# Kernel tuning notes

Measured on AMD Instinct MI355X. Metric: run time of the kernel, lower is better.

Reference implementation:

```python
import jax, jax.numpy as jnp
import numpy as np

DIM = 1024
N_HEADS = 16
HEAD_DIM = DIM // N_HEADS
LORA_DIM = 16
B, T = 4, 1024


def _rope(x):
    # x: [B, H, T, D] with D even; rotate first/second halves (torch impl style)
    D = x.shape[-1]
    half = D // 2
    theta = 1.0 / (10000.0 ** (jnp.arange(0, D, 2, dtype=jnp.float32) / D))  # [D/2]
    pos = jnp.arange(x.shape[-2], dtype=jnp.float32)                         # [T]
    pt = pos[:, None] * theta[None, :]                                       # [T, D/2]
    sin, cos = jnp.sin(pt), jnp.cos(pt)
    xr, xi = x[..., :half], x[..., half:]
    return jnp.concatenate([xr * cos - xi * sin, xr * sin + xi * cos], axis=-1)


def setup_inputs() -> dict:
    key = jax.random.key(0)
    ks = jax.random.split(key, 16)
    def n(k, shape, std=0.02):
        return jax.random.normal(k, shape, jnp.float32) * std
    return {
        "x": jax.random.normal(ks[0], (B, T, DIM), jnp.float32),
        "q_w": n(ks[1], (DIM, DIM)),
        "k_w": n(ks[2], (DIM, DIM)),
        "v_w": n(ks[3], (DIM, DIM)),
        "q_a": n(ks[4], (LORA_DIM, DIM), 0.001),
        "q_b": n(ks[5], (DIM, LORA_DIM), 0.001),
        "q_l": jax.random.normal(ks[6], (DIM,), jnp.float32),
        "k_a": n(ks[7], (LORA_DIM, DIM), 0.001),
        "k_b": n(ks[8], (DIM, LORA_DIM), 0.001),
        "k_l": jax.random.normal(ks[9], (DIM,), jnp.float32),
        "v_a": n(ks[10], (LORA_DIM, DIM), 0.001),
        "v_b": n(ks[11], (DIM, LORA_DIM), 0.001),
        "v_l": jax.random.normal(ks[12], (DIM,), jnp.float32),
        "proj_w": n(ks[13], (DIM, DIM)),
        "proj_b": n(ks[14], (DIM,)),
    }


def reference(x, q_w, k_w, v_w, q_a, q_b, q_l, k_a, k_b, k_l,
              v_a, v_b, v_l, proj_w, proj_b):
    Bb, Tt, C = x.shape
    # token shift: xx[t] = x[t-1], xx[0] = 0 (ZeroPad2d((0,0,1,-1)))
    xx = jnp.pad(x, ((0, 0), (1, 0), (0, 0)))[:, :Tt]
    xxx = xx - x

    def lora(a, b, lam):
        return lam + jnp.tanh(x @ a.T) @ b.T  # [B,T,C]

    q = (x + xxx * lora(q_a, q_b, q_l)) @ q_w.T
    k = (x + xxx * lora(k_a, k_b, k_l)) @ k_w.T
    v = (x + xxx * lora(v_a, v_b, v_l)) @ v_w.T

    def split_heads(t):
        return t.reshape(Bb, Tt, N_HEADS, HEAD_DIM).transpose(0, 2, 1, 3)  # [B,H,T,D]

    q = _rope(split_heads(q))
    k = _rope(split_heads(k))
    v = split_heads(v)

    scale = 1.0 / np.sqrt(HEAD_DIM).astype(np.float32)
    scores = jnp.einsum('bhqd,bhkd->bhqk', q, k) * scale
    causal = jnp.tril(jnp.ones((Tt, Tt), dtype=bool))
    scores = jnp.where(causal, scores, jnp.float32(-1e30))
    att = jax.nn.softmax(scores, axis=-1)
    out = jnp.einsum('bhqk,bhkd->bhqd', att, v)
    out = out.transpose(0, 2, 1, 3).reshape(Bb, Tt, C)
    return out @ proj_w.T + proj_b
```

## Files before the change

### kernel.cpp

```cpp
#include <hip/hip_runtime.h>
#include <hip/hip_bf16.h>

typedef __hip_bfloat16 bf16;
typedef __attribute__((ext_vector_type(8))) short bf16x8;
typedef __attribute__((ext_vector_type(4))) float f32x4;

typedef const __attribute__((address_space(1))) unsigned int* gp_t;
typedef __attribute__((address_space(3))) unsigned int* lp_t;

__device__ __forceinline__ bf16 tobf(float f) { return __float2bfloat16(f); }
__device__ __forceinline__ float tof(bf16 h) { return __bfloat162float(h); }

__device__ __forceinline__ short bfbits(float f) {
    bf16 h = __float2bfloat16(f);
    return *reinterpret_cast<short*>(&h);
}
__device__ __forceinline__ bf16x8 pack8(float4 a, float4 b) {
    bf16x8 r;
    r[0] = bfbits(a.x); r[1] = bfbits(a.y); r[2] = bfbits(a.z); r[3] = bfbits(a.w);
    r[4] = bfbits(b.x); r[5] = bfbits(b.y); r[6] = bfbits(b.z); r[7] = bfbits(b.w);
    return r;
}

__device__ __forceinline__ void gload_lds16(const void* g, void* l) {
    __builtin_amdgcn_global_load_lds((gp_t)g, (lp_t)l, 16, 0, 0);
}

__global__ __launch_bounds__(256) void convert_w(const float* qw, const float* kw,
                                                 const float* vw, const float* pw,
                                                 bf16* dst) {
    int m = blockIdx.y;
    const float* src = m == 0 ? qw : (m == 1 ? kw : (m == 2 ? vw : pw));
    bf16* d = dst + (size_t)m * (1u << 20);
    int i = (blockIdx.x * 256 + threadIdx.x) * 4;
    float4 f = *(const float4*)(src + i);
    d[i + 0] = tobf(f.x);
    d[i + 1] = tobf(f.y);
    d[i + 2] = tobf(f.z);
    d[i + 3] = tobf(f.w);
}

__global__ __launch_bounds__(256) void lora_gate_fused(
    const float* x,
    const float* qa, const float* ka, const float* va,
    const float* qbw, const float* ql,
    const float* kbw, const float* kl,
    const float* vbw, const float* vl,
    bf16* xqo, bf16* xko, bf16* xvo) {
    const int XS = 1028;
    int row0 = blockIdx.x * 16;
    int t0 = row0 & 1023;
    int tid = threadIdx.x;
    int wave = tid >> 6, lane = tid & 63;
    int quad = lane >> 4, l16 = lane & 15;

    __shared__ float sx[17 * 1028];
    __shared__ float sT[16 * 48];

    {
        int prow = (row0 == 0) ? 0 : row0 - 1;
        for (int i = 0; i < 17; ++i) {
            int grow = (i == 0) ? prow : row0 + i - 1;
            gload_lds16(x + (size_t)grow * 1024 + wave * 256 + lane * 4,
                        &sx[i * XS + wave * 256]);
        }
    }
    __syncthreads();

    if (wave < 3) {
        const float* am = wave == 0 ? qa : (wave == 1 ? ka : va);
        f32x4 acc = (f32x4){0.f, 0.f, 0.f, 0.f};
#pragma unroll 4
        for (int k0 = 0; k0 < 1024; k0 += 32) {
            const float* xs = &sx[(1 + l16) * XS + k0 + quad * 8];
            bf16x8 af = pack8(*(const float4*)xs, *(const float4*)(xs + 4));
            const float* as = am + (size_t)l16 * 1024 + k0 + quad * 8;
            bf16x8 bf_ = pack8(*(const float4*)as, *(const float4*)(as + 4));
            acc = __builtin_amdgcn_mfma_f32_16x16x32_bf16(af, bf_, acc, 0, 0, 0);
        }
#pragma unroll
        for (int r = 0; r < 4; ++r)
            sT[(quad * 4 + r) * 48 + wave * 16 + l16] = tanhf(acc[r]);
    }
    __syncthreads();

#pragma unroll
    for (int u = 0; u < 4; ++u) {
        int d = tid + u * 256;
        float qbv[16], kbv[16], vbv[16];
#pragma unroll
        for (int p = 0; p < 4; ++p) {
            *(float4*)&qbv[p * 4] = *(const float4*)(qbw + (size_t)d * 16 + p * 4);
            *(float4*)&kbv[p * 4] = *(const float4*)(kbw + (size_t)d * 16 + p * 4);
            *(float4*)&vbv[p * 4] = *(const float4*)(vbw + (size_t)d * 16 + p * 4);
        }
        float qlv = ql[d], klv = kl[d], vlv = vl[d];
        float xp = (t0 == 0) ? 0.f : sx[0 * XS + d];
        for (int rr = 0; rr < 16; ++rr) {
            float xc = sx[(rr + 1) * XS + d];
            float dx = xp - xc;
            float gq = qlv, gk = klv, gv = vlv;
#pragma unroll
            for (int j = 0; j < 16; ++j) {
                gq += sT[rr * 48 + j] * qbv[j];
                gk += sT[rr * 48 + 16 + j] * kbv[j];
                gv += sT[rr * 48 + 32 + j] * vbv[j];
            }
            size_t o = (size_t)(row0 + rr) * 1024 + d;
            xqo[o] = tobf(xc + dx * gq);
            xko[o] = tobf(xc + dx * gk);
            xvo[o] = tobf(xc + dx * gv);
            xp = xc;
        }
    }
}

__global__ __launch_bounds__(256) void gemm128(
    const bf16* A0, const bf16* A1, const bf16* A2,
    const bf16* W0, const bf16* W1, const bf16* W2,
    bf16* C0, bf16* C1, bf16* C2,
    const float* bias, float* outF, int proj, int zcnt) {
    const int K = 1024;
    int ppx = (zcnt * 32) >> 3;
    int xcd = blockIdx.x & 7;
    int j = blockIdx.x >> 3;
    int pair = xcd * ppx + (j >> 3);
    int n0 = (j & 7) * 128;
    int bz = pair >> 5;
    int m0 = (pair & 31) * 128;

    const bf16* A = bz == 0 ? A0 : (bz == 1 ? A1 : A2);
    const bf16* W = bz == 0 ? W0 : (bz == 1 ? W1 : W2);
    bf16* C = bz == 0 ? C0 : (bz == 1 ? C1 : C2);

    __shared__ alignas(16) bf16 sA[2][64 * 64];
    __shared__ alignas(16) bf16 sB[2][64 * 64];

    int wave = threadIdx.x >> 6, lane = threadIdx.x & 63;
    int quad = lane >> 4, l16 = lane & 15;

    f32x4 acc[4][4];
#pragma unroll
    for (int i = 0; i < 4; i++)
#pragma unroll
        for (int j2 = 0; j2 < 4; j2++) acc[i][j2] = (f32x4){0.f, 0.f, 0.f, 0.f};

    int Rb0 = wave * 16 + (lane >> 3);
    int s0 = lane & 7;

    auto stage = [&](int k0, int bufi) {
#pragma unroll
        for (int p = 0; p < 2; p++) {
            int R = Rb0 + p * 8;
            int cs = s0 ^ (R & 7);
            int mr = 2 * R + (cs >> 2);
            int kc = (cs & 3) * 8;
            gload_lds16(A + (size_t)(m0 + mr) * K + k0 + kc, &sA[bufi][(wave * 16 + p * 8) * 64]);
            gload_lds16(W + (size_t)(n0 + mr) * K + k0 + kc, &sB[bufi][(wave * 16 + p * 8) * 64]);
        }
    };

    int mw = (wave >> 1) * 64, nw = (wave & 1) * 64;
    int slot = (((l16 & 1) << 2) | quad) ^ ((l16 >> 1) & 7);
    int abase = ((mw >> 1) + (l16 >> 1)) * 64 + slot * 8;
    int bbase = ((nw >> 1) + (l16 >> 1)) * 64 + slot * 8;

    stage(0, 0);
    for (int it = 0; it < 32; ++it) {
        __syncthreads();
        if (it + 1 < 32) stage((it + 1) * 32, (it + 1) & 1);
        const bf16* pa = sA[it & 1];
        const bf16* pb = sB[it & 1];
        bf16x8 af[4], bfr[4];
#pragma unroll
        for (int f = 0; f < 4; f++) {
            af[f] = *(const bf16x8*)&pa[abase + f * 512];
            bfr[f] = *(const bf16x8*)&pb[bbase + f * 512];
        }
#pragma unroll
        for (int i = 0; i < 4; i++)
#pragma unroll
            for (int j2 = 0; j2 < 4; j2++)
                acc[i][j2] = __builtin_amdgcn_mfma_f32_16x16x32_bf16(af[i], bfr[j2], acc[i][j2], 0, 0, 0);
    }

    if (proj) {
#pragma unroll
        for (int i = 0; i < 4; i++) {
            int mrow = m0 + mw + i * 16 + quad * 4;
#pragma unroll
            for (int j2 = 0; j2 < 4; j2++) {
                int col = n0 + nw + j2 * 16 + l16;
                float bv = bias[col];
#pragma unroll
                for (int r = 0; r < 4; r++)
                    outF[(size_t)(mrow + r) * 1024 + col] = acc[i][j2][r] + bv;
            }
        }
    } else if (bz < 2) {
        float sc = (bz == 0) ? 0.125f : 1.0f;
#pragma unroll
        for (int i = 0; i < 4; i++) {
            int mrow = m0 + mw + i * 16 + quad * 4;
#pragma unroll
            for (int j2 = 0; j2 < 2; j2++) {
                int d = j2 * 16 + l16;
                float theta = __expf(-(float)d * (9.210340371976184f / 32.0f));
                int col = n0 + nw + j2 * 16 + l16;
#pragma unroll
                for (int r = 0; r < 4; r++) {
                    int t = (mrow + r) & 1023;
                    float s, c;
                    sincosf((float)t * theta, &s, &c);
                    float xr = acc[i][j2][r], xi = acc[i][j2 + 2][r];
                    C[(size_t)(mrow + r) * 1024 + col] = tobf((xr * c - xi * s) * sc);
                    C[(size_t)(mrow + r) * 1024 + col + 32] = tobf((xr * s + xi * c) * sc);
                }
            }
        }
    } else {
#pragma unroll
        for (int i = 0; i < 4; i++) {
            int mrow = m0 + mw + i * 16 + quad * 4;
#pragma unroll
            for (int j2 = 0; j2 < 4; j2++) {
                int col = n0 + nw + j2 * 16 + l16;
#pragma unroll
                for (int r = 0; r < 4; r++)
                    C[(size_t)(mrow + r) * 1024 + col] = tobf(acc[i][j2][r]);
            }
        }
    }
}

__global__ __launch_bounds__(256) void v_transpose(const bf16* v, bf16* Vt) {
    int bh = blockIdx.x, tblk = blockIdx.y;
    int b = bh >> 4, h = bh & 15;
    int t0 = tblk * 64;
    int tid = threadIdx.x;

    __shared__ bf16 sv[64 * 65];
    {
        int r = tid >> 2;
        int c0 = (tid & 3) * 16;
        size_t g = ((size_t)(b * 1024 + t0 + r)) * 1024 + h * 64 + c0;
#pragma unroll
        for (int u = 0; u < 16; u++) sv[(c0 + u) * 65 + r] = v[g + u];
    }
    __syncthreads();
    {
        int d = tid >> 2;
        int tc = (tid & 3) * 16;
        size_t g = ((size_t)(bh * 64 + d)) * 1024 + t0 + tc;
#pragma unroll
        for (int u = 0; u < 16; u++) Vt[g + u] = sv[d * 65 + tc + u];
    }
}

__global__ __launch_bounds__(256) void attention(const bf16* Qm, const bf16* Km,
                                                 const bf16* Vt, bf16* attn) {
    int gid = blockIdx.x;
    int qblk = 15 - (gid >> 6);
    int bh = (((gid >> 3) & 7) << 3) | (gid & 7);
    int b = bh >> 4, h = bh & 15;
    int wave = threadIdx.x >> 6, lane = threadIdx.x & 63;
    int quad = lane >> 4, l16 = lane & 15;
    int m7 = l16 & 7;

    const bf16* Qb = Qm + (size_t)b * 1024 * 1024 + h * 64;
    const bf16* Kb = Km + (size_t)b * 1024 * 1024 + h * 64;
    const bf16* Vb = Vt + (size_t)bh * 64 * 1024;

    __shared__ alignas(16) bf16 sK[2][64 * 64];
    __shared__ alignas(16) bf16 sV[2][64 * 64];
    __shared__ alignas(16) bf16 sP[4][16 * 64];

    int srow = lane >> 3;
    int scol = ((lane & 7) ^ srow) * 8;

    auto stage = [&](int kt, int bufi) {
#pragma unroll
        for (int p = 0; p < 2; p++) {
            int rbase = p * 32 + wave * 8;
            gload_lds16(Kb + (size_t)(kt * 64 + rbase + srow) * 1024 + scol, &sK[bufi][rbase * 64]);
            gload_lds16(Vb + (size_t)(rbase + srow) * 1024 + kt * 64 + scol, &sV[bufi][rbase * 64]);
        }
    };

    int qrow0 = qblk * 64 + wave * 16;
    bf16x8 aq0 = *(const bf16x8*)&Qb[(size_t)(qrow0 + l16) * 1024 + quad * 8];
    bf16x8 aq1 = *(const bf16x8*)&Qb[(size_t)(qrow0 + l16) * 1024 + quad * 8 + 32];

    f32x4 o[4];
#pragma unroll
    for (int nt = 0; nt < 4; nt++) o[nt] = (f32x4){0.f, 0.f, 0.f, 0.f};
    float mrow[4], lrow[4];
#pragma unroll
    for (int r = 0; r < 4; r++) { mrow[r] = -3.0e38f; lrow[r] = 0.f; }

    stage(0, 0);

    int buf = 0;
    for (int kt = 0; kt <= qblk; ++kt, buf ^= 1) {
        __syncthreads();
        if (kt < qblk) stage(kt + 1, buf ^ 1);

        f32x4 S[4];
#pragma unroll
        for (int j = 0; j < 4; j++) {
            int row = j * 16 + l16;
            bf16x8 bk0 = *(const bf16x8*)&sK[buf][row * 64 + ((quad ^ m7) * 8)];
            bf16x8 bk1 = *(const bf16x8*)&sK[buf][row * 64 + (((quad + 4) ^ m7) * 8)];
            f32x4 z = __builtin_amdgcn_mfma_f32_16x16x32_bf16(aq0, bk0, (f32x4){0.f, 0.f, 0.f, 0.f}, 0, 0, 0);
            S[j] = __builtin_amdgcn_mfma_f32_16x16x32_bf16(aq1, bk1, z, 0, 0, 0);
        }
        if (kt == qblk) {
#pragma unroll
            for (int j = 0; j < 4; j++) {
                int key = kt * 64 + j * 16 + l16;
#pragma unroll
                for (int r = 0; r < 4; r++) {
                    int qr = qrow0 + quad * 4 + r;
                    if (key > qr) S[j][r] = -3.0e38f;
                }
            }
        }
        float alpha[4];
#pragma unroll
        for (int r = 0; r < 4; r++) {
            float vmax = fmaxf(fmaxf(S[0][r], S[1][r]), fmaxf(S[2][r], S[3][r]));
            vmax = fmaxf(vmax, __shfl_xor(vmax, 1));
            vmax = fmaxf(vmax, __shfl_xor(vmax, 2));
            vmax = fmaxf(vmax, __shfl_xor(vmax, 4));
            vmax = fmaxf(vmax, __shfl_xor(vmax, 8));
            float mn = fmaxf(mrow[r], vmax);
            alpha[r] = __expf(mrow[r] - mn);
            mrow[r] = mn;
        }
        float rs[4] = {0.f, 0.f, 0.f, 0.f};
#pragma unroll
        for (int j = 0; j < 4; j++)
#pragma unroll
            for (int r = 0; r < 4; r++) {
                float p = __expf(S[j][r] - mrow[r]);
                S[j][r] = p;
                rs[r] += p;
            }
#pragma unroll
        for (int r = 0; r < 4; r++) {
            float v = rs[r];
            v += __shfl_xor(v, 1);
            v += __shfl_xor(v, 2);
            v += __shfl_xor(v, 4);
            v += __shfl_xor(v, 8);
            lrow[r] = lrow[r] * alpha[r] + v;
        }
#pragma unroll
        for (int nt = 0; nt < 4; nt++)
#pragma unroll
            for (int r = 0; r < 4; r++) o[nt][r] *= alpha[r];

#pragma unroll
        for (int j = 0; j < 4; j++) {
            int c = j * 2 + (l16 >> 3);
#pragma unroll
            for (int r = 0; r < 4; r++) {
                int prow = quad * 4 + r;
                sP[wave][prow * 64 + ((c ^ (prow & 7)) * 8) + m7] = tobf(S[j][r]);
            }
        }
        asm volatile("s_waitcnt lgkmcnt(0)" ::: "memory");
        bf16x8 ap0 = *(const bf16x8*)&sP[wave][l16 * 64 + ((quad ^ m7) * 8)];
        bf16x8 ap1 = *(const bf16x8*)&sP[wave][l16 * 64 + (((quad + 4) ^ m7) * 8)];
#pragma unroll
        for (int nt = 0; nt < 4; nt++) {
            int row = nt * 16 + l16;
            bf16x8 bv0 = *(const bf16x8*)&sV[buf][row * 64 + ((quad ^ m7) * 8)];
            bf16x8 bv1 = *(const bf16x8*)&sV[buf][row * 64 + (((quad + 4) ^ m7) * 8)];
            o[nt] = __builtin_amdgcn_mfma_f32_16x16x32_bf16(ap0, bv0, o[nt], 0, 0, 0);
            o[nt] = __builtin_amdgcn_mfma_f32_16x16x32_bf16(ap1, bv1, o[nt], 0, 0, 0);
        }
    }

    float invl[4];
#pragma unroll
    for (int r = 0; r < 4; r++) invl[r] = 1.0f / lrow[r];
#pragma unroll
    for (int nt = 0; nt < 4; nt++)
#pragma unroll
        for (int r = 0; r < 4; r++) {
            int t = qrow0 + quad * 4 + r;
            int col = h * 64 + nt * 16 + l16;
            attn[(size_t)(b * 1024 + t) * 1024 + col] = tobf(o[nt][r] * invl[r]);
        }
}

extern "C" void kernel_launch(void* const* d_in, const int* in_sizes, int n_in,
                              void* d_out, int out_size, void* d_ws, size_t ws_size,
                              hipStream_t stream) {
    const float* x = (const float*)d_in[0];
    const float* qw = (const float*)d_in[1];
    const float* kw = (const float*)d_in[2];
    const float* vw = (const float*)d_in[3];
    const float* qa = (const float*)d_in[4];
    const float* qb = (const float*)d_in[5];
    const float* ql = (const float*)d_in[6];
    const float* ka = (const float*)d_in[7];
    const float* kb = (const float*)d_in[8];
    const float* kl = (const float*)d_in[9];
    const float* va = (const float*)d_in[10];
    const float* vb = (const float*)d_in[11];
    const float* vl = (const float*)d_in[12];
    const float* pw = (const float*)d_in[13];
    const float* pb = (const float*)d_in[14];
    float* out = (float*)d_out;

    char* ws = (char*)d_ws;
    const size_t MB = 1024 * 1024;
    bf16* wqb = (bf16*)ws;
    bf16* wkb = wqb + 1048576;
    bf16* wvb = wkb + 1048576;
    bf16* wpb = wvb + 1048576;
    bf16* xqb = (bf16*)(ws + 8 * MB);
    bf16* xkb = xqb + 4194304;
    bf16* xvb = xkb + 4194304;
    bf16* qm = (bf16*)(ws + 32 * MB);
    bf16* km = qm + 4194304;
    bf16* vm = km + 4194304;
    bf16* Vt = xvb;
    bf16* attn = xqb;

    convert_w<<<dim3(1024, 4), 256, 0, stream>>>(qw, kw, vw, pw, wqb);
    lora_gate_fused<<<256, 256, 0, stream>>>(x, qa, ka, va, qb, ql, kb, kl, vb, vl,
                                             xqb, xkb, xvb);
    gemm128<<<768, 256, 0, stream>>>(xqb, xkb, xvb, wqb, wkb, wvb, qm, km, vm,
                                     nullptr, nullptr, 0, 3);
    v_transpose<<<dim3(64, 16), 256, 0, stream>>>(vm, Vt);
    attention<<<1024, 256, 0, stream>>>(qm, km, Vt, attn);
    gemm128<<<256, 256, 0, stream>>>(attn, nullptr, nullptr, wpb, nullptr, nullptr,
                                     nullptr, nullptr, nullptr, pb, out, 1, 1);
}
```

Baseline: 238.4 us.

## Single-buffer GEMM LDS staging and compute RoPE angles by incremental rotation

The GEMM mainloop drops its LDS double buffer: each iteration now loads a single tile and synchronises twice before computing, so global loads no longer overlap the MFMAs. The RoPE epilogue replaces a per-element sincosf with three sincosf calls per column, then advances the angle by angle-addition recurrences across rows. The recurrence saves transcendental work but lets rounding error build up over the steps. The single buffer halves LDS use, possibly raising occupancy, but exposes load latency.

```diff
diff --git a/kernel.cpp b/kernel.cpp
--- a/kernel.cpp
+++ b/kernel.cpp
@@ -133,8 +133,8 @@
     const bf16* W = bz == 0 ? W0 : (bz == 1 ? W1 : W2);
     bf16* C = bz == 0 ? C0 : (bz == 1 ? C1 : C2);
 
-    __shared__ alignas(16) bf16 sA[2][64 * 64];
-    __shared__ alignas(16) bf16 sB[2][64 * 64];
+    __shared__ alignas(16) bf16 sA[64 * 64];
+    __shared__ alignas(16) bf16 sB[64 * 64];
 
     int wave = threadIdx.x >> 6, lane = threadIdx.x & 63;
     int quad = lane >> 4, l16 = lane & 15;
@@ -148,15 +148,15 @@
     int Rb0 = wave * 16 + (lane >> 3);
     int s0 = lane & 7;
 
-    auto stage = [&](int k0, int bufi) {
+    auto stage = [&](int k0) {
 #pragma unroll
         for (int p = 0; p < 2; p++) {
             int R = Rb0 + p * 8;
             int cs = s0 ^ (R & 7);
             int mr = 2 * R + (cs >> 2);
             int kc = (cs & 3) * 8;
-            gload_lds16(A + (size_t)(m0 + mr) * K + k0 + kc, &sA[bufi][(wave * 16 + p * 8) * 64]);
-            gload_lds16(W + (size_t)(n0 + mr) * K + k0 + kc, &sB[bufi][(wave * 16 + p * 8) * 64]);
+            gload_lds16(A + (size_t)(m0 + mr) * K + k0 + kc, &sA[(wave * 16 + p * 8) * 64]);
+            gload_lds16(W + (size_t)(n0 + mr) * K + k0 + kc, &sB[(wave * 16 + p * 8) * 64]);
         }
     };
 
@@ -165,17 +165,15 @@
     int abase = ((mw >> 1) + (l16 >> 1)) * 64 + slot * 8;
     int bbase = ((nw >> 1) + (l16 >> 1)) * 64 + slot * 8;
 
-    stage(0, 0);
     for (int it = 0; it < 32; ++it) {
         __syncthreads();
-        if (it + 1 < 32) stage((it + 1) * 32, (it + 1) & 1);
-        const bf16* pa = sA[it & 1];
-        const bf16* pb = sB[it & 1];
+        stage(it * 32);
+        __syncthreads();
         bf16x8 af[4], bfr[4];
 #pragma unroll
         for (int f = 0; f < 4; f++) {
-            af[f] = *(const bf16x8*)&pa[abase + f * 512];
-            bfr[f] = *(const bf16x8*)&pb[bbase + f * 512];
+            af[f] = *(const bf16x8*)&sA[abase + f * 512];
+            bfr[f] = *(const bf16x8*)&sB[bbase + f * 512];
         }
 #pragma unroll
         for (int i = 0; i < 4; i++)
@@ -199,23 +197,32 @@
         }
     } else if (bz < 2) {
         float sc = (bz == 0) ? 0.125f : 1.0f;
-#pragma unroll
-        for (int i = 0; i < 4; i++) {
-            int mrow = m0 + mw + i * 16 + quad * 4;
-#pragma unroll
-            for (int j2 = 0; j2 < 2; j2++) {
-                int d = j2 * 16 + l16;
-                float theta = __expf(-(float)d * (9.210340371976184f / 32.0f));
-                int col = n0 + nw + j2 * 16 + l16;
+        int tb = ((m0 + mw) & 1023) + quad * 4;
+#pragma unroll
+        for (int j2 = 0; j2 < 2; j2++) {
+            int d = j2 * 16 + l16;
+            float theta = __expf(-(float)d * (9.210340371976184f / 32.0f));
+            float s1, c1, s16, c16, st, ct;
+            sincosf(theta, &s1, &c1);
+            sincosf(16.0f * theta, &s16, &c16);
+            sincosf((float)tb * theta, &st, &ct);
+            int col = n0 + nw + j2 * 16 + l16;
+#pragma unroll
+            for (int i = 0; i < 4; i++) {
+                int mrow = m0 + mw + i * 16 + quad * 4;
+                float c = ct, s = st;
 #pragma unroll
                 for (int r = 0; r < 4; r++) {
-                    int t = (mrow + r) & 1023;
-                    float s, c;
-                    sincosf((float)t * theta, &s, &c);
                     float xr = acc[i][j2][r], xi = acc[i][j2 + 2][r];
                     C[(size_t)(mrow + r) * 1024 + col] = tobf((xr * c - xi * s) * sc);
                     C[(size_t)(mrow + r) * 1024 + col + 32] = tobf((xr * s + xi * c) * sc);
+                    float cn = c * c1 - s * s1;
+                    s = s * c1 + c * s1;
+                    c = cn;
                 }
+                float cn = ct * c16 - st * s16;
+                st = st * c16 + ct * s16;
+                ct = cn;
             }
         }
     } else {
```

Measured after the change: 221.1 us. 1.08x faster.
